# Kernel optimization log

Measured on AMD Instinct MI355X. Metric: run time of the kernel, lower is better.

Reference implementation:

```python
import jax, jax.numpy as jnp
import numpy as np

B, N, T = 256, 512, 96
E, H, K = 8, 128, 2
PROB_THRESHOLD = 0.05
# SG auto-anneal: first forward sets temperature = t_max = 10.0 (cosine decay at step 0)
TEMP = 10.0


def setup_inputs() -> dict:
    key = jax.random.key(0)
    ks = jax.random.split(key, 8)
    s_g = 1.0 / np.sqrt(T)
    s_1 = 1.0 / np.sqrt(T)
    s_2 = 1.0 / np.sqrt(H)
    return {
        "x": jax.random.normal(ks[0], (B, N, T), dtype=jnp.float32),
        "Wg": jax.random.uniform(ks[1], (E, T), jnp.float32, -s_g, s_g),   # gate Linear(T, E)
        "bg": jax.random.uniform(ks[2], (E,), jnp.float32, -s_g, s_g),
        "W1": jax.random.uniform(ks[3], (E, T, H), jnp.float32, -s_1, s_1),  # stacked MLPExpert fc1
        "b1": jax.random.uniform(ks[4], (E, H), jnp.float32, -s_1, s_1),
        "W2": jax.random.uniform(ks[5], (E, H, T), jnp.float32, -s_2, s_2),  # stacked MLPExpert fc2
        "b2": jax.random.uniform(ks[6], (E, T), jnp.float32, -s_2, s_2),
        "route_scale": jnp.asarray(1.2, dtype=jnp.float32),
    }


def reference(x, Wg, bg, W1, b1, W2, b2, route_scale):
    b, n, t = x.shape
    BN = b * n
    xf = x.reshape(BN, t)                              # [BN, T]

    # ---- SG gate (eval mode: no noise; temp = t_max after first anneal step) ----
    logits = (xf @ Wg.T + bg) / TEMP                   # [BN, E]
    probs = jax.nn.softmax(logits, axis=-1)
    topw, topi = jax.lax.top_k(probs, K)               # [BN, K]
    w = topw / (jnp.sum(topw, axis=-1, keepdims=True) + 1e-12)  # topk_weights_norm

    # ---- SEA routing: capacity generous (never binds for this config); topk indices
    # are distinct so duplicate-expert reroute never triggers. Route is valid iff
    # normalized prob >= prob_threshold; invalid routes are passthrough (copy x). ----
    mask = w >= PROB_THRESHOLD                         # compute_mask [BN, K]

    # ---- SEE experts (MLPExpert with residual), computed densely per expert ----
    h = jax.nn.relu(jnp.einsum('bt,eth->ebh', xf, W1) + b1[:, None, :])   # [E, BN, H]
    y_all = jnp.einsum('ebh,eht->ebt', h, W2) + b2[:, None, :] + xf[None] # [E, BN, T]

    # gather each token's chosen expert outputs
    y_sel = y_all[topi, jnp.arange(BN)[:, None]]       # [BN, K, T]
    contrib = jnp.where(mask[..., None], y_sel, xf[:, None, :])

    # ---- weighted combine (SEE normalizes again, then scales) ----
    wn = w / jnp.clip(jnp.sum(w, axis=-1, keepdims=True), 1e-12)
    mixed = jnp.sum(contrib * wn[..., None], axis=1) * route_scale        # [BN, T]

    util = jnp.sum(mask[..., None] * jax.nn.one_hot(topi, E, dtype=xf.dtype), axis=1)
    return mixed.reshape(b, n, t), util.reshape(b, n, E)
```

## Files before the change

kernel.cpp:

```cpp
#include <hip/hip_runtime.h>
#include <hip/hip_bf16.h>

#define BN_TOTAL   131072
#define T_DIM      96
#define E_NUM      8
#define H_DIM      128
#define CAP        131072
#define PTHRESH    0.05f
#define NBLK       64

typedef _Float16 f16x8 __attribute__((ext_vector_type(8)));
typedef _Float16 f16x4 __attribute__((ext_vector_type(4)));
typedef float    f32x4 __attribute__((ext_vector_type(4)));

#define OFF_TOK    1024
#define OFF_SCALE  (OFF_TOK   + E_NUM * CAP * 4)
#define OFF_MASK   (OFF_SCALE + E_NUM * CAP * 4)
#define OFF_COEF   (OFF_MASK  + BN_TOTAL * 4)
#define OFF_YBUF   (OFF_COEF  + BN_TOTAL * 4)
#define OFF_XH     (OFF_YBUF + 2 * BN_TOTAL * T_DIM * 2)
#define OFF_W1T    (OFF_XH   + BN_TOTAL * T_DIM * 2)
#define OFF_W2T    (OFF_W1T  + E_NUM * H_DIM * T_DIM * 2)
#define WS_NEED    ((size_t)OFF_YBUF + (size_t)2 * BN_TOTAL * T_DIM * 4)


__global__ void zero_cnt_kernel(int* __restrict__ cnt) {
    if (threadIdx.x < E_NUM) cnt[threadIdx.x] = 0;
}

__global__ __launch_bounds__(256) void prep_kernel(
    const float* __restrict__ W1, const float* __restrict__ W2,
    _Float16* __restrict__ w1T, _Float16* __restrict__ w2T,
    int* __restrict__ cnt)
{
    __shared__ _Float16 tile[128 * 136];
    const int tid = threadIdx.x;
    if (blockIdx.x == 0 && tid < E_NUM) cnt[tid] = 0;
    const bool isW1 = blockIdx.x < 8;
    const int e = blockIdx.x & 7;
    const int R = isW1 ? T_DIM : H_DIM;
    const int C = isW1 ? H_DIM : T_DIM;
    const int S = isW1 ? 104 : 136;
    const float* src = (isW1 ? W1 : W2) + (size_t)e * T_DIM * H_DIM;
    _Float16* dst = (isW1 ? w1T : w2T) + (size_t)e * T_DIM * H_DIM;

    const int nb = (R >> 2) * (C >> 2);
    for (int b = tid; b < nb; b += 256) {
        const int r4 = b / (C >> 2), c4 = b % (C >> 2);
#pragma unroll
        for (int i = 0; i < 4; ++i) {
            const float4 v = *reinterpret_cast<const float4*>(src + (size_t)(4 * r4 + i) * C + 4 * c4);
            tile[(4 * c4 + 0) * S + 4 * r4 + i] = (_Float16)v.x;
            tile[(4 * c4 + 1) * S + 4 * r4 + i] = (_Float16)v.y;
            tile[(4 * c4 + 2) * S + 4 * r4 + i] = (_Float16)v.z;
            tile[(4 * c4 + 3) * S + 4 * r4 + i] = (_Float16)v.w;
        }
    }
    __syncthreads();
    const int chunks = C * (R >> 3);
    for (int q = tid; q < chunks; q += 256) {
        const int cr = q / (R >> 3), k = q % (R >> 3);
        *reinterpret_cast<f16x8*>(dst + (size_t)cr * R + 8 * k) =
            *reinterpret_cast<const f16x8*>(&tile[cr * S + 8 * k]);
    }
}

template<bool GATHER>
__global__ __launch_bounds__(1024) void gate_kernel(
    const float* __restrict__ x, const float* __restrict__ Wg,
    const float* __restrict__ bg, const float* __restrict__ rs_p,
    float* __restrict__ mixed, float* __restrict__ util,
    int* __restrict__ cnt, int* __restrict__ toklist, float* __restrict__ scalelist,
    int* __restrict__ maskbuf, float* __restrict__ coefbuf, _Float16* __restrict__ xh)
{
    __shared__ float wg_s[E_NUM][T_DIM];
    __shared__ float bg_s[E_NUM];
    __shared__ int wcnt[16][E_NUM];
    __shared__ int wbase[16][E_NUM];

    const int tid = threadIdx.x;
    for (int i = tid; i < E_NUM * T_DIM; i += 1024) wg_s[i / T_DIM][i % T_DIM] = Wg[i];
    if (tid < E_NUM) bg_s[tid] = bg[tid];
    __syncthreads();

    const int g   = tid >> 2;
    const int sub = tid & 3;
    const int token = blockIdx.x * 256 + g;
    const float* xr_f = x + (size_t)token * T_DIM + sub * 24;

    float4 xv[6];
#pragma unroll
    for (int i = 0; i < 6; ++i) xv[i] = reinterpret_cast<const float4*>(xr_f)[i];

    float logit[E_NUM];
#pragma unroll
    for (int e = 0; e < E_NUM; ++e) logit[e] = 0.0f;
#pragma unroll
    for (int i = 0; i < 6; ++i) {
#pragma unroll
        for (int e = 0; e < E_NUM; ++e) {
            const float4 wv = *reinterpret_cast<const float4*>(&wg_s[e][sub * 24 + 4 * i]);
            logit[e] = fmaf(xv[i].x, wv.x, logit[e]);
            logit[e] = fmaf(xv[i].y, wv.y, logit[e]);
            logit[e] = fmaf(xv[i].z, wv.z, logit[e]);
            logit[e] = fmaf(xv[i].w, wv.w, logit[e]);
        }
    }
#pragma unroll
    for (int e = 0; e < E_NUM; ++e) {
        logit[e] += __shfl_xor(logit[e], 1);
        logit[e] += __shfl_xor(logit[e], 2);
        logit[e] = (logit[e] + bg_s[e]) / 10.0f;
    }

    float mx = logit[0];
#pragma unroll
    for (int e = 1; e < E_NUM; ++e) mx = fmaxf(mx, logit[e]);
    float p[E_NUM]; float s = 0.0f;
#pragma unroll
    for (int e = 0; e < E_NUM; ++e) { p[e] = __expf(logit[e] - mx); s += p[e]; }
    const float inv_s = 1.0f / s;
#pragma unroll
    for (int e = 0; e < E_NUM; ++e) p[e] *= inv_s;

    int i0 = 0; float p0 = p[0];
#pragma unroll
    for (int e = 1; e < E_NUM; ++e) { if (p[e] > p0) { p0 = p[e]; i0 = e; } }
    int i1 = -1; float p1 = -1.0f;
#pragma unroll
    for (int e = 0; e < E_NUM; ++e) { if (e != i0 && p[e] > p1) { p1 = p[e]; i1 = e; } }

    const float denom0 = p0 + p1 + 1e-12f;
    const float w0 = p0 / denom0, w1 = p1 / denom0;
    const bool m0 = (w0 >= PTHRESH), m1 = (w1 >= PTHRESH);
    const float sumw = w0 + w1;
    const float denom1 = fmaxf(sumw, 1e-12f);
    const float wn0 = w0 / denom1, wn1 = w1 / denom1;
    const float rs = *rs_p;
    const float coef = rs * (wn0 + wn1);
    const bool lead = (sub == 0);

    const int lane = tid & 63;
    const int wv_id = tid >> 6;
    const unsigned long long lt = (1ULL << lane) - 1ULL;

    int wcnt_mine = 0, offA = 0, offB = 0;
#pragma unroll
    for (int e = 0; e < E_NUM; ++e) {
        const unsigned long long A = __ballot(lead && m0 && (i0 == e));
        const unsigned long long B = __ballot(lead && m1 && (i1 == e));
        const int na = __popcll(A), nb = __popcll(B);
        if (lane == e) wcnt_mine = na + nb;
        if (lead && m0 && (i0 == e)) offA = __popcll(A & lt);
        if (lead && m1 && (i1 == e)) offB = na + __popcll(B & lt);
    }
    if (lane < E_NUM) wcnt[wv_id][lane] = wcnt_mine;
    __syncthreads();

    int run = 0, c[16];
    if (tid < E_NUM) {
        int tot = 0;
#pragma unroll
        for (int w = 0; w < 16; ++w) { c[w] = wcnt[w][tid]; tot += c[w]; }
        run = atomicAdd(&cnt[tid], tot);
    }

    if (GATHER) {
        _Float16* xr = xh + (size_t)token * T_DIM + sub * 24;
#pragma unroll
        for (int i = 0; i < 6; ++i) {
            f16x4 h4;
            h4[0] = (_Float16)xv[i].x; h4[1] = (_Float16)xv[i].y;
            h4[2] = (_Float16)xv[i].z; h4[3] = (_Float16)xv[i].w;
            reinterpret_cast<f16x4*>(xr)[i] = h4;
        }
        if (lead) { coefbuf[token] = coef; maskbuf[token] = (m0 ? 1 : 0) | (m1 ? 2 : 0); }
    } else {
        float* mr = mixed + (size_t)token * T_DIM + sub * 24;
#pragma unroll
        for (int i = 0; i < 6; ++i)
            reinterpret_cast<float4*>(mr)[i] =
                make_float4(coef * xv[i].x, coef * xv[i].y, coef * xv[i].z, coef * xv[i].w);
    }
    if (lead) {
        float u[E_NUM];
#pragma unroll
        for (int e = 0; e < E_NUM; ++e)
            u[e] = (((e == i0) && m0) || ((e == i1) && m1)) ? 1.0f : 0.0f;
        float4* u4 = reinterpret_cast<float4*>(util + (size_t)token * E_NUM);
        u4[0] = make_float4(u[0], u[1], u[2], u[3]);
        u4[1] = make_float4(u[4], u[5], u[6], u[7]);
    }

    if (tid < E_NUM) {
#pragma unroll
        for (int w = 0; w < 16; ++w) { wbase[w][tid] = run; run += c[w]; }
    }
    __syncthreads();

    if (lead && m0) {
        const int pos = wbase[wv_id][i0] + offA;
        toklist[i0 * CAP + pos] = (token << 1);
        scalelist[i0 * CAP + pos] = rs * wn0;
    }
    if (lead && m1) {
        const int pos = wbase[wv_id][i1] + offB;
        toklist[i1 * CAP + pos] = (token << 1) | 1;
        scalelist[i1 * CAP + pos] = rs * wn1;
    }
}

template<bool GATHER>
__global__ __launch_bounds__(256, 2) void expert_kernel(
    const float* __restrict__ x, const _Float16* __restrict__ xh,
    const float* __restrict__ W1, const float* __restrict__ b1,
    const float* __restrict__ W2, const float* __restrict__ b2,
    const _Float16* __restrict__ w1T, const _Float16* __restrict__ w2T,
    float* __restrict__ mixed, _Float16* __restrict__ ybh,
    const int* __restrict__ cnt, const int* __restrict__ toklist,
    const float* __restrict__ scalelist)
{
    __shared__ __align__(16) _Float16 Hs[2][64 * 136];

    const int e = blockIdx.y;
    const int count = cnt[e];
    if ((int)blockIdx.x * 64 >= count) return;

    const int tid  = threadIdx.x;
    const int w    = tid >> 6;
    const int lane = tid & 63;
    const int lm   = lane & 15;
    const int lg4  = lane >> 4;
    const int mhalf = w & 1;
    const int nhalf = w >> 1;

    const int*   tl = toklist   + (size_t)e * CAP;
    const float* sl = scalelist + (size_t)e * CAP;

    f16x8 w1f[3][4];
    {
        const _Float16* w1e = w1T + (size_t)e * H_DIM * T_DIM;
        const float*    gW1 = W1  + (size_t)e * T_DIM * H_DIM;
#pragma unroll
        for (int ks = 0; ks < 3; ++ks)
#pragma unroll
            for (int n = 0; n < 4; ++n) {
                const int h = nhalf * 64 + n * 16 + lm;
                if (GATHER) {
                    w1f[ks][n] = *reinterpret_cast<const f16x8*>(
                        w1e + (size_t)h * T_DIM + ks * 32 + lg4 * 8);
                } else {
                    f16x8 v;
#pragma unroll
                    for (int j = 0; j < 8; ++j)
                        v[j] = (_Float16)gW1[(size_t)(ks * 32 + lg4 * 8 + j) * H_DIM + h];
                    w1f[ks][n] = v;
                }
            }
    }
    f16x8 w2f[4][3];
    {
        const _Float16* w2e = w2T + (size_t)e * H_DIM * T_DIM;
        const float*    gW2 = W2  + (size_t)e * H_DIM * T_DIM;
#pragma unroll
        for (int ks = 0; ks < 4; ++ks)
#pragma unroll
            for (int n = 0; n < 3; ++n) {
                const int t = nhalf * 48 + n * 16 + lm;
                if (GATHER) {
                    w2f[ks][n] = *reinterpret_cast<const f16x8*>(
                        w2e + (size_t)t * H_DIM + ks * 32 + lg4 * 8);
                } else {
                    f16x8 v;
#pragma unroll
                    for (int j = 0; j < 8; ++j)
                        v[j] = (_Float16)gW2[(size_t)(ks * 32 + lg4 * 8 + j) * T_DIM + t];
                    w2f[ks][n] = v;
                }
            }
    }
    float4 b1v[4], b2v[3];
#pragma unroll
    for (int n = 0; n < 4; ++n)
        b1v[n] = *reinterpret_cast<const float4*>(b1 + e * H_DIM + nhalf * 64 + n * 16 + lg4 * 4);
#pragma unroll
    for (int n = 0; n < 3; ++n)
        b2v[n] = *reinterpret_cast<const float4*>(b2 + e * T_DIM + nhalf * 48 + n * 16 + lg4 * 4);

    int buf = 0;
    for (int t0 = blockIdx.x * 64; t0 < count; t0 += NBLK * 64) {
        const int nt = min(64, count - t0);

        int packedi[2]; float sci[2]; bool val[2]; int rowi[2];
#pragma unroll
        for (int mt = 0; mt < 2; ++mt) {
            const int slot = (mhalf * 2 + mt) * 16 + lm;
            val[mt] = slot < nt;
            const int gi = t0 + (val[mt] ? slot : 0);
            packedi[mt] = tl[gi];
            rowi[mt] = packedi[mt] >> 1;
            sci[mt] = sl[gi];
        }

        f16x8 xf[2][3];
#pragma unroll
        for (int mt = 0; mt < 2; ++mt)
#pragma unroll
            for (int ks = 0; ks < 3; ++ks) {
                if (GATHER) {
                    xf[mt][ks] = *reinterpret_cast<const f16x8*>(
                        xh + (size_t)rowi[mt] * T_DIM + ks * 32 + lg4 * 8);
                } else {
                    const float* xp = x + (size_t)rowi[mt] * T_DIM + ks * 32 + lg4 * 8;
                    f16x8 v;
#pragma unroll
                    for (int j = 0; j < 8; ++j) v[j] = (_Float16)xp[j];
                    xf[mt][ks] = v;
                }
            }

        f32x4 acc1[2][4];
#pragma unroll
        for (int mt = 0; mt < 2; ++mt)
#pragma unroll
            for (int n = 0; n < 4; ++n) acc1[mt][n] = f32x4{0.f, 0.f, 0.f, 0.f};
#pragma unroll
        for (int ks = 0; ks < 3; ++ks)
#pragma unroll
            for (int n = 0; n < 4; ++n) {
                acc1[0][n] = __builtin_amdgcn_mfma_f32_16x16x32_f16(w1f[ks][n], xf[0][ks], acc1[0][n], 0, 0, 0);
                acc1[1][n] = __builtin_amdgcn_mfma_f32_16x16x32_f16(w1f[ks][n], xf[1][ks], acc1[1][n], 0, 0, 0);
            }

#pragma unroll
        for (int mt = 0; mt < 2; ++mt) {
            const int tok = (mhalf * 2 + mt) * 16 + lm;
#pragma unroll
            for (int n = 0; n < 4; ++n) {
                const float* bb = reinterpret_cast<const float*>(&b1v[n]);
                f16x4 hv;
#pragma unroll
                for (int r = 0; r < 4; ++r)
                    hv[r] = (_Float16)fmaxf(acc1[mt][n][r] + bb[r], 0.0f);
                *reinterpret_cast<f16x4*>(&Hs[buf][tok * 136 + nhalf * 64 + n * 16 + lg4 * 4]) = hv;
            }
        }
        __syncthreads();

        f32x4 acc2[2][3];
#pragma unroll
        for (int mt = 0; mt < 2; ++mt)
#pragma unroll
            for (int n = 0; n < 3; ++n) acc2[mt][n] = f32x4{0.f, 0.f, 0.f, 0.f};
#pragma unroll
        for (int ks = 0; ks < 4; ++ks) {
            const f16x8 hf0 = *reinterpret_cast<const f16x8*>(
                &Hs[buf][((mhalf * 2 + 0) * 16 + lm) * 136 + ks * 32 + lg4 * 8]);
            const f16x8 hf1 = *reinterpret_cast<const f16x8*>(
                &Hs[buf][((mhalf * 2 + 1) * 16 + lm) * 136 + ks * 32 + lg4 * 8]);
#pragma unroll
            for (int n = 0; n < 3; ++n) {
                acc2[0][n] = __builtin_amdgcn_mfma_f32_16x16x32_f16(w2f[ks][n], hf0, acc2[0][n], 0, 0, 0);
                acc2[1][n] = __builtin_amdgcn_mfma_f32_16x16x32_f16(w2f[ks][n], hf1, acc2[1][n], 0, 0, 0);
            }
        }

#pragma unroll
        for (int mt = 0; mt < 2; ++mt) {
            if (val[mt]) {
#pragma unroll
                for (int n = 0; n < 3; ++n) {
                    const float* bb = reinterpret_cast<const float*>(&b2v[n]);
                    f16x4 yv;
#pragma unroll
                    for (int r = 0; r < 4; ++r)
                        yv[r] = (_Float16)(sci[mt] * (acc2[mt][n][r] + bb[r]));
                    if (GATHER) {
                        *reinterpret_cast<f16x4*>(
                            ybh + (size_t)packedi[mt] * T_DIM + nhalf * 48 + n * 16 + lg4 * 4) = yv;
                    } else {
#pragma unroll
                        for (int r = 0; r < 4; ++r)
                            atomicAdd(&mixed[(size_t)(packedi[mt] >> 1) * T_DIM +
                                             nhalf * 48 + n * 16 + lg4 * 4 + r], (float)yv[r]);
                    }
                }
            }
        }
        buf ^= 1;
    }
}

__global__ __launch_bounds__(256) void finalize_kernel(
    const _Float16* __restrict__ xh, const _Float16* __restrict__ ybh,
    const int* __restrict__ maskbuf, const float* __restrict__ coefbuf,
    float* __restrict__ mixed)
{
    const int tid = threadIdx.x;
    const int token = blockIdx.x * 32 + (tid >> 3);
    const int seg = (tid & 7) * 12;

    const float coef = coefbuf[token];
    const int mask = maskbuf[token];

    const f16x4* xs = reinterpret_cast<const f16x4*>(xh + (size_t)token * T_DIM + seg);
    float4* od = reinterpret_cast<float4*>(mixed + (size_t)token * T_DIM + seg);

    float4 r[3];
#pragma unroll
    for (int q = 0; q < 3; ++q) {
        const f16x4 xv = xs[q];
        r[q] = make_float4(coef * (float)xv[0], coef * (float)xv[1],
                           coef * (float)xv[2], coef * (float)xv[3]);
    }
    if (mask & 1) {
        const f16x4* ys = reinterpret_cast<const f16x4*>(ybh + (size_t)(2 * token) * T_DIM + seg);
#pragma unroll
        for (int q = 0; q < 3; ++q) {
            const f16x4 yv = ys[q];
            r[q].x += (float)yv[0]; r[q].y += (float)yv[1];
            r[q].z += (float)yv[2]; r[q].w += (float)yv[3];
        }
    }
    if (mask & 2) {
        const f16x4* ys = reinterpret_cast<const f16x4*>(ybh + (size_t)(2 * token + 1) * T_DIM + seg);
#pragma unroll
        for (int q = 0; q < 3; ++q) {
            const f16x4 yv = ys[q];
            r[q].x += (float)yv[0]; r[q].y += (float)yv[1];
            r[q].z += (float)yv[2]; r[q].w += (float)yv[3];
        }
    }
#pragma unroll
    for (int q = 0; q < 3; ++q) od[q] = r[q];
}

extern "C" void kernel_launch(void* const* d_in, const int* in_sizes, int n_in,
                              void* d_out, int out_size, void* d_ws, size_t ws_size,
                              hipStream_t stream)
{
    const float* x  = (const float*)d_in[0];
    const float* Wg = (const float*)d_in[1];
    const float* bg = (const float*)d_in[2];
    const float* W1 = (const float*)d_in[3];
    const float* b1 = (const float*)d_in[4];
    const float* W2 = (const float*)d_in[5];
    const float* b2 = (const float*)d_in[6];
    const float* rs = (const float*)d_in[7];

    float* mixed = (float*)d_out;
    float* util  = mixed + (size_t)BN_TOTAL * T_DIM;

    char* ws = (char*)d_ws;
    int*      cnt       = (int*)ws;
    int*      toklist   = (int*)(ws + OFF_TOK);
    float*    scalelist = (float*)(ws + OFF_SCALE);
    int*      maskbuf   = (int*)(ws + OFF_MASK);
    float*    coefbuf   = (float*)(ws + OFF_COEF);
    _Float16* ybh       = (_Float16*)(ws + OFF_YBUF);
    _Float16* xh        = (_Float16*)(ws + OFF_XH);
    _Float16* w1T       = (_Float16*)(ws + OFF_W1T);
    _Float16* w2T       = (_Float16*)(ws + OFF_W2T);

    const bool gather = (ws_size >= WS_NEED);

    if (gather) {
        prep_kernel<<<16, 256, 0, stream>>>(W1, W2, w1T, w2T, cnt);
        gate_kernel<true><<<BN_TOTAL / 256, 1024, 0, stream>>>(
            x, Wg, bg, rs, mixed, util, cnt, toklist, scalelist, maskbuf, coefbuf, xh);
        expert_kernel<true><<<dim3(NBLK, E_NUM), 256, 0, stream>>>(
            x, xh, W1, b1, W2, b2, w1T, w2T, mixed, ybh, cnt, toklist, scalelist);
        finalize_kernel<<<BN_TOTAL / 32, 256, 0, stream>>>(
            xh, ybh, maskbuf, coefbuf, mixed);
    } else {
        zero_cnt_kernel<<<1, 64, 0, stream>>>(cnt);
        gate_kernel<false><<<BN_TOTAL / 256, 1024, 0, stream>>>(
            x, Wg, bg, rs, mixed, util, cnt, toklist, scalelist, maskbuf, coefbuf, xh);
        expert_kernel<false><<<dim3(NBLK, E_NUM), 256, 0, stream>>>(
            x, xh, W1, b1, W2, b2, w1T, w2T, mixed, ybh, cnt, toklist, scalelist);
    }
}
```

Baseline: 94.76 us.

## Stage expert weights in LDS instead of registers, single-buffer H tile

Expert W1/W2 fragments now live in shared memory, loaded once per block, instead of being held in per-thread registers (24 f16x8 values). The double-buffered H tile becomes a single buffer with an added barrier after the second GEMM. The aim is to cut VGPR pressure and possibly raise occupancy. In exchange, each MFMA now needs an extra LDS read, and each loop iteration pays an extra __syncthreads.

Measured after the change: 97.79 us. 1.03x slower.

```diff
diff --git a/kernel.cpp b/kernel.cpp
--- a/kernel.cpp
+++ b/kernel.cpp
@@ -220,7 +220,9 @@
     const int* __restrict__ cnt, const int* __restrict__ toklist,
     const float* __restrict__ scalelist)
 {
-    __shared__ __align__(16) _Float16 Hs[2][64 * 136];
+    __shared__ __align__(16) _Float16 w1Ls[H_DIM * 104];
+    __shared__ __align__(16) _Float16 w2Ls[T_DIM * 136];
+    __shared__ __align__(16) _Float16 Hs[64 * 136];
 
     const int e = blockIdx.y;
     const int count = cnt[e];
@@ -237,47 +239,30 @@
     const int*   tl = toklist   + (size_t)e * CAP;
     const float* sl = scalelist + (size_t)e * CAP;
 
-    f16x8 w1f[3][4];
-    {
+    if (GATHER) {
         const _Float16* w1e = w1T + (size_t)e * H_DIM * T_DIM;
-        const float*    gW1 = W1  + (size_t)e * T_DIM * H_DIM;
-#pragma unroll
-        for (int ks = 0; ks < 3; ++ks)
-#pragma unroll
-            for (int n = 0; n < 4; ++n) {
-                const int h = nhalf * 64 + n * 16 + lm;
-                if (GATHER) {
-                    w1f[ks][n] = *reinterpret_cast<const f16x8*>(
-                        w1e + (size_t)h * T_DIM + ks * 32 + lg4 * 8);
-                } else {
-                    f16x8 v;
-#pragma unroll
-                    for (int j = 0; j < 8; ++j)
-                        v[j] = (_Float16)gW1[(size_t)(ks * 32 + lg4 * 8 + j) * H_DIM + h];
-                    w1f[ks][n] = v;
-                }
-            }
-    }
-    f16x8 w2f[4][3];
-    {
+        for (int q = tid; q < 1536; q += 256) {
+            const int h = q / 12, cch = q % 12;
+            *reinterpret_cast<f16x8*>(&w1Ls[h * 104 + cch * 8]) =
+                *reinterpret_cast<const f16x8*>(&w1e[h * T_DIM + cch * 8]);
+        }
         const _Float16* w2e = w2T + (size_t)e * H_DIM * T_DIM;
-        const float*    gW2 = W2  + (size_t)e * H_DIM * T_DIM;
-#pragma unroll
-        for (int ks = 0; ks < 4; ++ks)
-#pragma unroll
-            for (int n = 0; n < 3; ++n) {
-                const int t = nhalf * 48 + n * 16 + lm;
-                if (GATHER) {
-                    w2f[ks][n] = *reinterpret_cast<const f16x8*>(
-                        w2e + (size_t)t * H_DIM + ks * 32 + lg4 * 8);
-                } else {
-                    f16x8 v;
-#pragma unroll
-                    for (int j = 0; j < 8; ++j)
-                        v[j] = (_Float16)gW2[(size_t)(ks * 32 + lg4 * 8 + j) * T_DIM + t];
-                    w2f[ks][n] = v;
-                }
-            }
+        for (int q = tid; q < 1536; q += 256) {
+            const int t = q / 16, cch = q % 16;
+            *reinterpret_cast<f16x8*>(&w2Ls[t * 136 + cch * 8]) =
+                *reinterpret_cast<const f16x8*>(&w2e[t * H_DIM + cch * 8]);
+        }
+    } else {
+        const float* gW1 = W1 + (size_t)e * T_DIM * H_DIM;
+        for (int q = tid; q < H_DIM * T_DIM; q += 256) {
+            const int h = q / T_DIM, t = q % T_DIM;
+            w1Ls[h * 104 + t] = (_Float16)gW1[(size_t)t * H_DIM + h];
+        }
+        const float* gW2 = W2 + (size_t)e * H_DIM * T_DIM;
+        for (int q = tid; q < H_DIM * T_DIM; q += 256) {
+            const int t = q / H_DIM, h = q % H_DIM;
+            w2Ls[t * 136 + h] = (_Float16)gW2[(size_t)h * T_DIM + t];
+        }
     }
     float4 b1v[4], b2v[3];
 #pragma unroll
@@ -286,8 +271,8 @@
 #pragma unroll
     for (int n = 0; n < 3; ++n)
         b2v[n] = *reinterpret_cast<const float4*>(b2 + e * T_DIM + nhalf * 48 + n * 16 + lg4 * 4);
-
-    int buf = 0;
+    __syncthreads();
+
     for (int t0 = blockIdx.x * 64; t0 < count; t0 += NBLK * 64) {
         const int nt = min(64, count - t0);
 
@@ -328,8 +313,10 @@
         for (int ks = 0; ks < 3; ++ks)
 #pragma unroll
             for (int n = 0; n < 4; ++n) {
-                acc1[0][n] = __builtin_amdgcn_mfma_f32_16x16x32_f16(w1f[ks][n], xf[0][ks], acc1[0][n], 0, 0, 0);
-                acc1[1][n] = __builtin_amdgcn_mfma_f32_16x16x32_f16(w1f[ks][n], xf[1][ks], acc1[1][n], 0, 0, 0);
+                const f16x8 wa = *reinterpret_cast<const f16x8*>(
+                    &w1Ls[(nhalf * 64 + n * 16 + lm) * 104 + ks * 32 + lg4 * 8]);
+                acc1[0][n] = __builtin_amdgcn_mfma_f32_16x16x32_f16(wa, xf[0][ks], acc1[0][n], 0, 0, 0);
+                acc1[1][n] = __builtin_amdgcn_mfma_f32_16x16x32_f16(wa, xf[1][ks], acc1[1][n], 0, 0, 0);
             }
 
 #pragma unroll
@@ -342,7 +329,7 @@
 #pragma unroll
                 for (int r = 0; r < 4; ++r)
                     hv[r] = (_Float16)fmaxf(acc1[mt][n][r] + bb[r], 0.0f);
-                *reinterpret_cast<f16x4*>(&Hs[buf][tok * 136 + nhalf * 64 + n * 16 + lg4 * 4]) = hv;
+                *reinterpret_cast<f16x4*>(&Hs[tok * 136 + nhalf * 64 + n * 16 + lg4 * 4]) = hv;
             }
         }
         __syncthreads();
@@ -355,15 +342,18 @@
 #pragma unroll
         for (int ks = 0; ks < 4; ++ks) {
             const f16x8 hf0 = *reinterpret_cast<const f16x8*>(
-                &Hs[buf][((mhalf * 2 + 0) * 16 + lm) * 136 + ks * 32 + lg4 * 8]);
+                &Hs[((mhalf * 2 + 0) * 16 + lm) * 136 + ks * 32 + lg4 * 8]);
             const f16x8 hf1 = *reinterpret_cast<const f16x8*>(
-                &Hs[buf][((mhalf * 2 + 1) * 16 + lm) * 136 + ks * 32 + lg4 * 8]);
+                &Hs[((mhalf * 2 + 1) * 16 + lm) * 136 + ks * 32 + lg4 * 8]);
 #pragma unroll
             for (int n = 0; n < 3; ++n) {
-                acc2[0][n] = __builtin_amdgcn_mfma_f32_16x16x32_f16(w2f[ks][n], hf0, acc2[0][n], 0, 0, 0);
-                acc2[1][n] = __builtin_amdgcn_mfma_f32_16x16x32_f16(w2f[ks][n], hf1, acc2[1][n], 0, 0, 0);
+                const f16x8 wb = *reinterpret_cast<const f16x8*>(
+                    &w2Ls[(nhalf * 48 + n * 16 + lm) * 136 + ks * 32 + lg4 * 8]);
+                acc2[0][n] = __builtin_amdgcn_mfma_f32_16x16x32_f16(wb, hf0, acc2[0][n], 0, 0, 0);
+                acc2[1][n] = __builtin_amdgcn_mfma_f32_16x16x32_f16(wb, hf1, acc2[1][n], 0, 0, 0);
             }
         }
+        __syncthreads();
 
 #pragma unroll
         for (int mt = 0; mt < 2; ++mt) {
@@ -387,7 +377,6 @@
                 }
             }
         }
-        buf ^= 1;
     }
 }
 
```
